# Optimization experiments

Measured on AMD Instinct MI355X. Metric: run time of the kernel, lower is better.

The kernel has to match this reference:

```python
import jax, jax.numpy as jnp
import numpy as np

NH, KVH, HD = 32, 8, 128          # num heads, kv heads, head dim
HIDDEN = NH * HD                   # 4096
K_BITS = V_BITS = 4
GROUP = 32                         # quantization group size
THETA = 10000.0
FEAT = 32 // K_BITS                # values packed per int32


def _rope_cos_sin(pos, dtype=jnp.float32):
    inv_freq = 1.0 / (THETA ** (jnp.arange(0, HD, 2, dtype=jnp.float32) / HD))
    freqs = pos.astype(jnp.float32)[:, None] * inv_freq[None, :]
    emb = jnp.concatenate([freqs, freqs], axis=-1)  # [t, HD]
    return jnp.cos(emb).astype(dtype), jnp.sin(emb).astype(dtype)


def _rotate_half(x):
    x1, x2 = jnp.split(x, 2, axis=-1)
    return jnp.concatenate([-x2, x1], axis=-1)


def _apply_rope(x, pos):  # x: [b, h, t, d], pos: [t]
    cos, sin = _rope_cos_sin(pos, x.dtype)
    return x * cos[None, None] + _rotate_half(x) * sin[None, None]


def _unpack(packed, bits):
    # packed int32 [..., n] -> float [..., n * (32//bits)], little-endian bit fields
    feat = 32 // bits
    shifts = jnp.arange(feat, dtype=jnp.int32) * bits
    vals = (packed[..., None] >> shifts) & ((1 << bits) - 1)
    return vals.reshape(packed.shape[:-1] + (packed.shape[-1] * feat,)).astype(jnp.float32)


def _dequant(packed, scale, mn, bits, group):
    # group-wise affine dequant: x = q * scale + mn along last dim
    qv = _unpack(packed, bits)
    lead, L = qv.shape[:-1], qv.shape[-1]
    qv = qv.reshape(lead + (L // group, group))
    return (qv * scale[..., None] + mn[..., None]).reshape(lead + (L,))


def _repeat_kv(x, n):
    return jnp.repeat(x, n, axis=1)


def setup_inputs() -> dict:
    key = jax.random.key(0)
    ks = jax.random.split(key, 13)
    B, QL = 8, 8
    TQ, FULL_PAST = 3968, 56
    s = 0.02
    return {
        "hidden_states": jax.random.normal(ks[0], (B, QL, HIDDEN), jnp.float32),
        "Wq": jax.random.normal(ks[1], (NH * HD, HIDDEN), jnp.float32) * s,
        "Wk": jax.random.normal(ks[2], (KVH * HD, HIDDEN), jnp.float32) * s,
        "Wv": jax.random.normal(ks[3], (KVH * HD, HIDDEN), jnp.float32) * s,
        "Wo": jax.random.normal(ks[4], (NH * HD, NH * HD), jnp.float32) * s,
        "key_quant_trans": jax.random.randint(ks[5], (B, KVH, HD, TQ // FEAT), 0, 2**31 - 1, jnp.int32),
        "key_scale_trans": jax.random.uniform(ks[6], (B, KVH, HD, TQ // GROUP), jnp.float32) * 0.05 + 0.01,
        "key_mn_trans": jax.random.normal(ks[7], (B, KVH, HD, TQ // GROUP), jnp.float32) * 0.1,
        "key_full_past": jax.random.normal(ks[8], (B, KVH, FULL_PAST, HD), jnp.float32),
        "value_quant": jax.random.randint(ks[9], (B, KVH, TQ, HD // FEAT), 0, 2**31 - 1, jnp.int32),
        "value_scale": jax.random.uniform(ks[10], (B, KVH, TQ, HD // GROUP), jnp.float32) * 0.05 + 0.01,
        "value_mn": jax.random.normal(ks[11], (B, KVH, TQ, HD // GROUP), jnp.float32) * 0.1,
        "value_full_past": jax.random.normal(ks[12], (B, KVH, FULL_PAST, HD), jnp.float32),
    }


def reference(hidden_states, Wq, Wk, Wv, Wo,
              key_quant_trans, key_scale_trans, key_mn_trans, key_full_past,
              value_quant, value_scale, value_mn, value_full_past):
    b, q_len, _ = hidden_states.shape
    groups = NH // KVH
    # projections
    q = (hidden_states @ Wq.T).reshape(b, q_len, NH, HD).transpose(0, 2, 1, 3)
    k = (hidden_states @ Wk.T).reshape(b, q_len, KVH, HD).transpose(0, 2, 1, 3)
    v = (hidden_states @ Wv.T).reshape(b, q_len, KVH, HD).transpose(0, 2, 1, 3)

    TQ = key_quant_trans.shape[-1] * FEAT
    past_len = TQ + key_full_past.shape[2]
    pos_new = jnp.arange(past_len, past_len + q_len)
    qr = _apply_rope(q, pos_new)

    # quantized key segment: dequant (stored transposed [b,kvh,HD,TQ]) + fused RoPE + bmm
    kq = _dequant(key_quant_trans, key_scale_trans, key_mn_trans, K_BITS, GROUP)
    kq = _apply_rope(kq.transpose(0, 1, 3, 2), jnp.arange(TQ))  # [b,kvh,TQ,HD]
    att_quant = jnp.einsum('bhqd,bhkd->bhqk', qr, _repeat_kv(kq, groups))

    # full-precision residual key segment
    k_full = jnp.concatenate([key_full_past, k], axis=2)
    pos_full = jnp.arange(past_len + q_len - k_full.shape[2], past_len + q_len)
    k_full = _apply_rope(k_full, pos_full)
    att_full = jnp.einsum('bhqd,bhkd->bhqk', qr, _repeat_kv(k_full, groups))

    attn = jnp.concatenate([att_quant, att_full], axis=-1) / np.sqrt(HD).astype(np.float32)
    attn = jax.nn.softmax(attn.astype(jnp.float32), axis=-1).astype(qr.dtype)

    # quantized values (packed along head_dim) + full residual values
    vq = _dequant(value_quant, value_scale, value_mn, V_BITS, GROUP)  # [b,kvh,TQ,HD]
    v_full = jnp.concatenate([value_full_past, v], axis=2)
    Lf = v_full.shape[2]
    out = jnp.einsum('bhqk,bhkd->bhqd', attn[..., :-Lf], _repeat_kv(vq, groups)) \
        + jnp.einsum('bhqk,bhkd->bhqd', attn[..., -Lf:], _repeat_kv(v_full, groups))

    out = out.transpose(0, 2, 1, 3).reshape(b, q_len, NH * HD)
    return out @ Wo.T
```

## Files before the change

kernel.cpp:

```cpp
#include <hip/hip_runtime.h>

typedef unsigned short u16;
typedef short bf16x8 __attribute__((ext_vector_type(8)));
typedef float f32x4 __attribute__((ext_vector_type(4)));

__device__ __forceinline__ float b2f(u16 u){ return __uint_as_float(((unsigned)u)<<16); }
__device__ __forceinline__ u16 f2bf(float f){ return (u16)((__float_as_uint(f)+0x8000u)>>16); }
__device__ __forceinline__ float ldf(const void* p, int i, bool isbf){
  return isbf ? b2f(((const u16*)p)[i]) : ((const float*)p)[i];
}
__device__ __forceinline__ float2 ld2(const void* p, int i, bool isbf){
  if (isbf) { unsigned u = *(const unsigned*)((const u16*)p + i);
              return make_float2(b2f((u16)(u & 0xffffu)), b2f((u16)(u >> 16))); }
  return *(const float2*)((const float*)p + i);
}
__device__ __forceinline__ void ld8(u16* dst, const void* p, int i, bool isbf){
  if (isbf) { *(uint4*)dst = *(const uint4*)((const u16*)p + i); }
  else {
    float4 a = *(const float4*)((const float*)p + i);
    float4 b = *(const float4*)((const float*)p + i + 4);
    dst[0]=f2bf(a.x); dst[1]=f2bf(a.y); dst[2]=f2bf(a.z); dst[3]=f2bf(a.w);
    dst[4]=f2bf(b.x); dst[5]=f2bf(b.y); dst[6]=f2bf(b.z); dst[7]=f2bf(b.w);
  }
}
__device__ __forceinline__ float c8(const float* __restrict__ p, int i, int stride){
  float s = 0.f;
  #pragma unroll
  for (int k = 0; k < 8; k++) s += p[i + k*stride];
  return s;
}
__device__ __forceinline__ void bar(){ asm volatile("s_waitcnt lgkmcnt(0)\n\ts_barrier" ::: "memory"); }
#define MFMA16(a,b,c) __builtin_amdgcn_mfma_f32_16x16x32_bf16((a),(b),(c),0,0,0)

__global__ __launch_bounds__(256) void ctab_kernel(const u16* __restrict__ h,
                                                   int* __restrict__ flag,
                                                   float2* __restrict__ ctab) {
  int tid = threadIdx.x;
  if (blockIdx.x == 0) {
    int cnt = 0;
    for (int i = tid; i < 4096; i += 256) {
      int e = (h[i] >> 7) & 0xFF;
      cnt += (e >= 116 && e <= 132) ? 1 : 0;
    }
    __shared__ int sh[256];
    sh[tid] = cnt; __syncthreads();
    for (int s = 128; s > 0; s >>= 1) { if (tid < s) sh[tid] += sh[tid + s]; __syncthreads(); }
    if (tid == 0) flag[0] = (sh[0] >= 3100) ? 1 : 0;
  }
  int idx = blockIdx.x * 256 + tid;
  int dm = idx & 63, t = idx >> 6;
  float f = exp2f(-(float)dm * (13.287712379549449f / 64.0f));
  float ang = (float)t * f;
  float s, c;
  sincosf(ang, &s, &c);
  ctab[idx] = make_float2(c, s);
}

__global__ __launch_bounds__(256) void proj_kernel(
    const void* __restrict__ X, const void* __restrict__ Wa,
    const void* __restrict__ Wb, const void* __restrict__ Wc,
    float* __restrict__ out32, int Na, int Nb, int ostride,
    const int* __restrict__ flagp, int x_dyn)
{
  bool fbf = (*flagp != 0);
  bool xbf = x_dyn ? fbf : true;
  int n0 = blockIdx.x * 32;
  int ks0 = blockIdx.y * 512;
  const void* W; int wr0;
  if (n0 < Na)           { W = Wa; wr0 = n0; }
  else if (n0 < Na + Nb) { W = Wb; wr0 = n0 - Na; }
  else                   { W = Wc; wr0 = n0 - Na - Nb; }

  __shared__ u16 Xs[64][136];
  __shared__ u16 Ws[32][136];
  int tid = threadIdx.x;
  int wv = tid >> 6, lane = tid & 63, lr = lane & 15, lq = lane >> 4;
  f32x4 acc0 = {0.f,0.f,0.f,0.f}, acc1 = {0.f,0.f,0.f,0.f};

  for (int ki = 0; ki < 4; ki++) {
    int k0 = ks0 + ki * 128;
    __syncthreads();
    for (int u = tid; u < 1024; u += 256) {
      int row = u >> 4, cc = u & 15;
      ld8(&Xs[row][cc * 8], X, row * 4096 + k0 + cc * 8, xbf);
    }
    for (int u = tid; u < 512; u += 256) {
      int row = u >> 4, cc = u & 15;
      ld8(&Ws[row][cc * 8], W, (wr0 + row) * 4096 + k0 + cc * 8, fbf);
    }
    __syncthreads();
    #pragma unroll
    for (int ks = 0; ks < 4; ks++) {
      bf16x8 af = *(const bf16x8*)&Xs[wv * 16 + lr][ks * 32 + lq * 8];
      bf16x8 b0 = *(const bf16x8*)&Ws[lr][ks * 32 + lq * 8];
      bf16x8 b1 = *(const bf16x8*)&Ws[16 + lr][ks * 32 + lq * 8];
      acc0 = MFMA16(af, b0, acc0);
      acc1 = MFMA16(af, b1, acc1);
    }
  }
  float* outp = out32 + (size_t)blockIdx.y * 64 * ostride;
  #pragma unroll
  for (int r = 0; r < 4; r++) {
    outp[(wv * 16 + lq * 4 + r) * ostride + n0 + lr]      = acc0[r];
    outp[(wv * 16 + lq * 4 + r) * ostride + n0 + 16 + lr] = acc1[r];
  }
}

__global__ __launch_bounds__(256) void prep_kernel(
    const float* __restrict__ Cq32, const void* __restrict__ kfp, const void* __restrict__ vfp,
    const float2* __restrict__ ctab, const int* __restrict__ flagp,
    u16* __restrict__ qrb, u16* __restrict__ kfullb, u16* __restrict__ vfullT)
{
  bool isbf = (*flagp != 0);
  int idx = blockIdx.x * 256 + threadIdx.x;
  if (idx < 262144) {
    int d = idx & 127, row = (idx >> 7) & 31, bh = idx >> 12;
    int b = bh >> 3, kvh = bh & 7, g = row >> 3, qp = row & 7;
    int tok = b * 8 + qp, h = kvh * 4 + g;
    float x  = c8(Cq32, tok * 6144 + h * 128 + d, 393216);
    float x2 = c8(Cq32, tok * 6144 + h * 128 + (d ^ 64), 393216);
    float2 cs = ctab[(4024 + qp) * 64 + (d & 63)];
    float sgn = (d < 64) ? -1.f : 1.f;
    qrb[idx] = f2bf(x * cs.x + sgn * (x2 * cs.y));
  } else if (idx < 786432) {
    int j = idx - 262144;
    int d = j & 127, t = (j >> 7) & 63, bh = j >> 13;
    int b = bh >> 3, kvh = bh & 7;
    float x, x2;
    if (t < 56) {
      x  = ldf(kfp, (bh * 56 + t) * 128 + d, isbf);
      x2 = ldf(kfp, (bh * 56 + t) * 128 + (d ^ 64), isbf);
    } else {
      int tok = b * 8 + (t - 56);
      x  = c8(Cq32, tok * 6144 + 4096 + kvh * 128 + d, 393216);
      x2 = c8(Cq32, tok * 6144 + 4096 + kvh * 128 + (d ^ 64), 393216);
    }
    float2 cs = ctab[(3968 + t) * 64 + (d & 63)];
    float sgn = (d < 64) ? -1.f : 1.f;
    kfullb[j] = f2bf(x * cs.x + sgn * (x2 * cs.y));
  } else {
    int j = idx - 786432;
    int t = j & 63, d = (j >> 6) & 127, bh = j >> 13;
    int b = bh >> 3, kvh = bh & 7;
    float x;
    if (t < 56) x = ldf(vfp, (bh * 56 + t) * 128 + d, isbf);
    else        x = c8(Cq32, (b * 8 + t - 56) * 6144 + 5120 + kvh * 128 + d, 393216);
    vfullT[j] = f2bf(x);
  }
}

__global__ __launch_bounds__(256) void attn_kernel(
    const int* __restrict__ kqw, const void* __restrict__ ksc, const void* __restrict__ kmn,
    const int* __restrict__ vqw, const void* __restrict__ vsc, const void* __restrict__ vmn,
    const u16* __restrict__ qrb, const u16* __restrict__ kfullb, const u16* __restrict__ vfullT,
    const float2* __restrict__ ctab, const int* __restrict__ flagp,
    u16* __restrict__ Opart, float* __restrict__ ml)
{
  bool isbf = (*flagp != 0);
  int bh = blockIdx.x, grp = blockIdx.y;
  int tid = threadIdx.x;

  __shared__ __align__(16) unsigned char L[23552];
  u16 (*Ktile)[136] = (u16(*)[136])L;
  u16 (*Vtile)[72]  = (u16(*)[72])L;
  u16 (*Pl)[72] = (u16(*)[72])(L + 18432);
  float* pmax = (float*)(L + 23040);
  float* psum = (float*)(L + 23296);

  int wv = tid >> 6, lane = tid & 63, lr = lane & 15, lq = lane >> 4;
  int mt = wv & 1, nh = wv >> 1;

  const int* kq_lo = kqw + (bh * 128 + lane) * 496;
  const int* kq_hi = kq_lo + 64 * 496;
  int klo = (bh * 128 + lane) * 124;
  int khi = klo + 64 * 124;
  const int* vqp = vqw + (bh * 3968 + lane) * 16 + wv * 4;
  int voff = (bh * 3968 + lane) * 4 + wv;

  bf16x8 qa[4];
  #pragma unroll
  for (int ks = 0; ks < 4; ks++)
    qa[ks] = *(const bf16x8*)&qrb[(bh * 32 + mt * 16 + lr) * 128 + ks * 32 + lq * 8];

  unsigned kwl[2], kwh[2];
  float2 ksl, kml, ksh, kmh;
  uint4 vw;
  float vs, vm;
  {
    int c0 = grp * 4;
    kwl[0] = kq_lo[c0 * 8 + wv]; kwl[1] = kq_lo[c0 * 8 + wv + 4];
    kwh[0] = kq_hi[c0 * 8 + wv]; kwh[1] = kq_hi[c0 * 8 + wv + 4];
    ksl = ld2(ksc, klo + c0 * 2, isbf); kml = ld2(kmn, klo + c0 * 2, isbf);
    ksh = ld2(ksc, khi + c0 * 2, isbf); kmh = ld2(kmn, khi + c0 * 2, isbf);
    vw = *(const uint4*)(vqp + c0 * 1024);
    vs = ldf(vsc, voff + c0 * 256, isbf); vm = ldf(vmn, voff + c0 * 256, isbf);
  }

  float m_prev[4], l_run[4];
  #pragma unroll
  for (int r = 0; r < 4; r++) { m_prev[r] = -INFINITY; l_run[r] = 0.f; }
  f32x4 zf = {0.f,0.f,0.f,0.f};
  f32x4 oacc[4] = {zf, zf, zf, zf};

  for (int j = 0; j < 4; j++) {
    int c = grp * 4 + j;
    if (c >= 63) break;
    bool fullc = (c == 62);
    bool pf = (j < 3) && (c + 1 < 62);

    bar();
    if (!fullc) {
      #pragma unroll
      for (int it = 0; it < 2; it++) {
        int w = wv + 4 * it;
        unsigned w1 = kwl[it], w2 = kwh[it];
        float sc1 = it ? ksl.y : ksl.x, m1 = it ? kml.y : kml.x;
        float sc2 = it ? ksh.y : ksh.x, m2 = it ? kmh.y : kmh.x;
        const float2* ct = &ctab[(c * 64 + w * 8) * 64 + lane];
        #pragma unroll
        for (int i = 0; i < 8; i++) {
          float v1 = (float)((w1 >> (4 * i)) & 15u) * sc1 + m1;
          float v2 = (float)((w2 >> (4 * i)) & 15u) * sc2 + m2;
          float2 cs = ct[i * 64];
          Ktile[w * 8 + i][lane]      = f2bf(v1 * cs.x - v2 * cs.y);
          Ktile[w * 8 + i][lane + 64] = f2bf(v2 * cs.x + v1 * cs.y);
        }
      }
    } else {
      for (int u = tid; u < 1024; u += 256) {
        int row = u >> 4, cc = u & 15;
        *(uint4*)&Ktile[row][cc * 8] = *(const uint4*)&kfullb[(bh * 64 + row) * 128 + cc * 8];
      }
    }
    if (pf) {
      int cn = c + 1;
      kwl[0] = kq_lo[cn * 8 + wv]; kwl[1] = kq_lo[cn * 8 + wv + 4];
      kwh[0] = kq_hi[cn * 8 + wv]; kwh[1] = kq_hi[cn * 8 + wv + 4];
      ksl = ld2(ksc, klo + cn * 2, isbf); kml = ld2(kmn, klo + cn * 2, isbf);
      ksh = ld2(ksc, khi + cn * 2, isbf); kmh = ld2(kmn, khi + cn * 2, isbf);
    }
    bar();
    f32x4 sacc[2] = {zf, zf};
    #pragma unroll
    for (int ks = 0; ks < 4; ks++) {
      #pragma unroll
      for (int nt = 0; nt < 2; nt++) {
        bf16x8 bfr = *(const bf16x8*)&Ktile[nh * 32 + nt * 16 + lr][ks * 32 + lq * 8];
        sacc[nt] = MFMA16(qa[ks], bfr, sacc[nt]);
      }
    }
    float mx[4];
    #pragma unroll
    for (int r = 0; r < 4; r++) {
      sacc[0][r] *= 0.08838834764831845f;
      sacc[1][r] *= 0.08838834764831845f;
      mx[r] = fmaxf(sacc[0][r], sacc[1][r]);
    }
    #pragma unroll
    for (int m = 1; m < 16; m <<= 1) {
      #pragma unroll
      for (int r = 0; r < 4; r++) mx[r] = fmaxf(mx[r], __shfl_xor(mx[r], m));
    }
    if (lr == 0) {
      #pragma unroll
      for (int r = 0; r < 4; r++) pmax[wv * 16 + lq * 4 + r] = mx[r];
    }
    bar();
    if (!fullc) {
      unsigned wds[4] = {vw.x, vw.y, vw.z, vw.w};
      #pragma unroll
      for (int it = 0; it < 4; it++) {
        int w = wv * 4 + it;
        unsigned wd = wds[it];
        #pragma unroll
        for (int i = 0; i < 8; i++)
          Vtile[w * 8 + i][lane] = f2bf((float)((wd >> (4 * i)) & 15u) * vs + vm);
      }
    } else {
      for (int u = tid; u < 1024; u += 256) {
        int dd = u >> 3, t8 = u & 7;
        *(uint4*)&Vtile[dd][t8 * 8] = *(const uint4*)&vfullT[(bh * 128 + dd) * 64 + t8 * 8];
      }
    }
    if (pf) {
      int cn = c + 1;
      vw = *(const uint4*)(vqp + cn * 1024);
      vs = ldf(vsc, voff + cn * 256, isbf); vm = ldf(vmn, voff + cn * 256, isbf);
    }
    float alpha[4], osum[4];
    #pragma unroll
    for (int r = 0; r < 4; r++) {
      float cm = fmaxf(mx[r], pmax[(wv ^ 2) * 16 + lq * 4 + r]);
      float mn2 = fmaxf(m_prev[r], cm);
      alpha[r] = __expf(m_prev[r] - mn2);
      m_prev[r] = mn2;
    }
    u16 pb[2][4];
    #pragma unroll
    for (int r = 0; r < 4; r++) {
      float p0 = __expf(sacc[0][r] - m_prev[r]);
      float p1 = __expf(sacc[1][r] - m_prev[r]);
      pb[0][r] = f2bf(p0); pb[1][r] = f2bf(p1);
      osum[r] = b2f(pb[0][r]) + b2f(pb[1][r]);
    }
    #pragma unroll
    for (int m = 1; m < 16; m <<= 1) {
      #pragma unroll
      for (int r = 0; r < 4; r++) osum[r] += __shfl_xor(osum[r], m);
    }
    #pragma unroll
    for (int nt = 0; nt < 2; nt++)
      #pragma unroll
      for (int r = 0; r < 4; r++)
        Pl[mt * 16 + lq * 4 + r][nh * 32 + nt * 16 + lr] = pb[nt][r];
    if (lr == 0) {
      #pragma unroll
      for (int r = 0; r < 4; r++) psum[wv * 16 + lq * 4 + r] = osum[r];
    }
    bar();
    f32x4 pv[4] = {zf, zf, zf, zf};
    #pragma unroll
    for (int ks = 0; ks < 2; ks++) {
      bf16x8 af = *(const bf16x8*)&Pl[mt * 16 + lr][ks * 32 + lq * 8];
      #pragma unroll
      for (int nt = 0; nt < 4; nt++) {
        bf16x8 bfr = *(const bf16x8*)&Vtile[nh * 64 + nt * 16 + lr][ks * 32 + lq * 8];
        pv[nt] = MFMA16(af, bfr, pv[nt]);
      }
    }
    #pragma unroll
    for (int r = 0; r < 4; r++)
      l_run[r] = l_run[r] * alpha[r] + osum[r] + psum[(wv ^ 2) * 16 + lq * 4 + r];
    #pragma unroll
    for (int nt = 0; nt < 4; nt++)
      #pragma unroll
      for (int r = 0; r < 4; r++)
        oacc[nt][r] = oacc[nt][r] * alpha[r] + pv[nt][r];
  }

  u16* Ob = Opart + (size_t)((bh * 16 + grp) * 32) * 128;
  #pragma unroll
  for (int nt = 0; nt < 4; nt++)
    #pragma unroll
    for (int r = 0; r < 4; r++)
      Ob[(mt * 16 + lq * 4 + r) * 128 + nh * 64 + nt * 16 + lr] = f2bf(oacc[nt][r]);
  if (wv < 2 && lr == 0) {
    #pragma unroll
    for (int r = 0; r < 4; r++) {
      ml[((bh * 16 + grp) * 32 + mt * 16 + lq * 4 + r) * 2 + 0] = m_prev[r];
      ml[((bh * 16 + grp) * 32 + mt * 16 + lq * 4 + r) * 2 + 1] = l_run[r];
    }
  }
}

__global__ __launch_bounds__(256) void combine_kernel(
    const u16* __restrict__ Opart, const float* __restrict__ ml, u16* __restrict__ attn_out)
{
  int bh = blockIdx.x, dq = blockIdx.y, tid = threadIdx.x;
  __shared__ float Wg[16][33];
  __shared__ float Ls[32];
  if (tid < 32) {
    int row = tid;
    float M = -INFINITY;
    for (int g = 0; g < 16; g++)
      M = fmaxf(M, ml[((bh * 16 + g) * 32 + row) * 2]);
    float Lacc = 0.f;
    for (int g = 0; g < 16; g++) {
      float m = ml[((bh * 16 + g) * 32 + row) * 2];
      float l = ml[((bh * 16 + g) * 32 + row) * 2 + 1];
      float w = __expf(m - M);
      Wg[g][row] = w;
      Lacc += l * w;
    }
    Ls[row] = Lacc;
  }
  __syncthreads();
  int row = tid >> 3, ds = tid & 7;
  int d0 = dq * 32 + ds * 4;
  float a0 = 0.f, a1 = 0.f, a2 = 0.f, a3 = 0.f;
  for (int g = 0; g < 16; g++) {
    float w = Wg[g][row];
    const u16* p = Opart + (size_t)((bh * 16 + g) * 32 + row) * 128 + d0;
    uint2 v = *(const uint2*)p;
    const u16* h = (const u16*)&v;
    a0 += w * b2f(h[0]); a1 += w * b2f(h[1]); a2 += w * b2f(h[2]); a3 += w * b2f(h[3]);
  }
  float inv = 1.0f / Ls[row];
  int b = bh >> 3, kvh = bh & 7, hg = row >> 3, qp = row & 7;
  u16* dst = attn_out + (size_t)(b * 8 + qp) * 4096 + (kvh * 4 + hg) * 128 + d0;
  dst[0] = f2bf(a0 * inv); dst[1] = f2bf(a1 * inv);
  dst[2] = f2bf(a2 * inv); dst[3] = f2bf(a3 * inv);
}

__global__ __launch_bounds__(256) void cast_kernel(
    const float* __restrict__ O32, const int* __restrict__ flagp, void* __restrict__ out)
{
  int i = blockIdx.x * 256 + threadIdx.x;
  float v = c8(O32, i, 262144);
  if (*flagp) ((u16*)out)[i] = f2bf(v);
  else        ((float*)out)[i] = v;
}

extern "C" void kernel_launch(void* const* d_in, const int* in_sizes, int n_in,
                              void* d_out, int out_size, void* d_ws, size_t ws_size,
                              hipStream_t stream)
{
  const void* hidden = d_in[0];
  const void* Wq  = d_in[1];
  const void* Wk  = d_in[2];
  const void* Wv  = d_in[3];
  const void* Wo  = d_in[4];
  const int*  kqw = (const int*)d_in[5];
  const void* ksc = d_in[6];
  const void* kmn = d_in[7];
  const void* kfp = d_in[8];
  const int*  vqw = (const int*)d_in[9];
  const void* vsc = d_in[10];
  const void* vmn = d_in[11];
  const void* vfp = d_in[12];

  char* ws = (char*)d_ws;
  int*    flag     = (int*)(ws);
  float2* ctab     = (float2*)(ws + 256);
  float*  Cq32     = (float*)(ws + 2064640);
  u16*    Opart    = (u16*)(ws + 2064640);
  float*  O32      = (float*)(ws + 2064640);
  u16*    qrb      = (u16*)(ws + 18841856);
  u16*    attn_out = qrb;
  u16*    kfullb   = (u16*)(ws + 19366144);
  u16*    vfullT   = (u16*)(ws + 20414720);
  float*  ml       = (float*)(ws + 21463296);

  ctab_kernel<<<1008, 256, 0, stream>>>((const u16*)hidden, flag, ctab);
  proj_kernel<<<dim3(192, 8), 256, 0, stream>>>(hidden, Wq, Wk, Wv, Cq32, 4096, 1024, 6144, flag, 1);
  prep_kernel<<<5120, 256, 0, stream>>>(Cq32, kfp, vfp, ctab, flag, qrb, kfullb, vfullT);
  attn_kernel<<<dim3(64, 16), 256, 0, stream>>>(kqw, ksc, kmn, vqw, vsc, vmn,
                                                qrb, kfullb, vfullT, ctab, flag, Opart, ml);
  combine_kernel<<<dim3(64, 4), 256, 0, stream>>>(Opart, ml, attn_out);
  proj_kernel<<<dim3(128, 8), 256, 0, stream>>>(attn_out, Wo, Wo, Wo, O32, 4096, 0, 4096, flag, 0);
  cast_kernel<<<1024, 256, 0, stream>>>(O32, flag, d_out);
}
```

Before: 316.9 us.

## Software-pipeline attention chunks with separate K/V/P LDS tiles and swizzle

Restructures the attention loop so the PV matmul of the previous chunk overlaps with the QK of the current one. K, V and P now have separate XOR-swizzled LDS buffers, which cuts barriers per chunk and avoids bank conflicts. The row sum now comes from an MFMA against a ones vector rather than shuffle reductions, and the row max uses DPP row-rotates. It also sets launch bounds for 4 blocks per CU. The cost is more LDS per block (37 KB) and more live registers, which could limit occupancy.

```diff
diff --git a/kernel.cpp b/kernel.cpp
--- a/kernel.cpp
+++ b/kernel.cpp
@@ -30,6 +30,8 @@
   return s;
 }
 __device__ __forceinline__ void bar(){ asm volatile("s_waitcnt lgkmcnt(0)\n\ts_barrier" ::: "memory"); }
+#define RORMAX(x, ctrl) fmaxf((x), __int_as_float(__builtin_amdgcn_update_dpp( \
+    __float_as_int(x), __float_as_int(x), (ctrl), 0xF, 0xF, false)))
 #define MFMA16(a,b,c) __builtin_amdgcn_mfma_f32_16x16x32_bf16((a),(b),(c),0,0,0)
 
 __global__ __launch_bounds__(256) void ctab_kernel(const u16* __restrict__ h,
@@ -149,7 +151,7 @@
   }
 }
 
-__global__ __launch_bounds__(256) void attn_kernel(
+__global__ __launch_bounds__(256, 4) void attn_kernel(
     const int* __restrict__ kqw, const void* __restrict__ ksc, const void* __restrict__ kmn,
     const int* __restrict__ vqw, const void* __restrict__ vsc, const void* __restrict__ vmn,
     const u16* __restrict__ qrb, const u16* __restrict__ kfullb, const u16* __restrict__ vfullT,
@@ -159,16 +161,18 @@
   bool isbf = (*flagp != 0);
   int bh = blockIdx.x, grp = blockIdx.y;
   int tid = threadIdx.x;
-
-  __shared__ __align__(16) unsigned char L[23552];
-  u16 (*Ktile)[136] = (u16(*)[136])L;
-  u16 (*Vtile)[72]  = (u16(*)[72])L;
-  u16 (*Pl)[72] = (u16(*)[72])(L + 18432);
-  float* pmax = (float*)(L + 23040);
-  float* psum = (float*)(L + 23296);
+  int c0 = grp * 4;
+  int N = (grp == 15) ? 3 : 4;
+
+  __shared__ __align__(16) unsigned char L[37120];
+  u16* Kt = (u16*)L;
+  u16* Vt = (u16*)(L + 16384);
+  u16* Pt = (u16*)(L + 32768);
+  float* pmax = (float*)(L + 36864);
 
   int wv = tid >> 6, lane = tid & 63, lr = lane & 15, lq = lane >> 4;
   int mt = wv & 1, nh = wv >> 1;
+  int sx = (lr & 7) << 3;
 
   const int* kq_lo = kqw + (bh * 128 + lane) * 496;
   const int* kq_hi = kq_lo + 64 * 496;
@@ -181,113 +185,101 @@
   #pragma unroll
   for (int ks = 0; ks < 4; ks++)
     qa[ks] = *(const bf16x8*)&qrb[(bh * 32 + mt * 16 + lr) * 128 + ks * 32 + lq * 8];
+  bf16x8 onev;
+  #pragma unroll
+  for (int j2 = 0; j2 < 8; j2++) onev[j2] = (short)0x3F80;
+
+  float m_prev[4], l_run[4], alpha[4], mx[4];
+  f32x4 zf = {0.f,0.f,0.f,0.f};
+  f32x4 oacc[4] = {zf, zf, zf, zf};
+  f32x4 sacc[2];
+  #pragma unroll
+  for (int r = 0; r < 4; r++) { m_prev[r] = -INFINITY; l_run[r] = 0.f; }
 
   unsigned kwl[2], kwh[2];
   float2 ksl, kml, ksh, kmh;
-  uint4 vw;
-  float vs, vm;
-  {
-    int c0 = grp * 4;
-    kwl[0] = kq_lo[c0 * 8 + wv]; kwl[1] = kq_lo[c0 * 8 + wv + 4];
-    kwh[0] = kq_hi[c0 * 8 + wv]; kwh[1] = kq_hi[c0 * 8 + wv + 4];
-    ksl = ld2(ksc, klo + c0 * 2, isbf); kml = ld2(kmn, klo + c0 * 2, isbf);
-    ksh = ld2(ksc, khi + c0 * 2, isbf); kmh = ld2(kmn, khi + c0 * 2, isbf);
-    vw = *(const uint4*)(vqp + c0 * 1024);
-    vs = ldf(vsc, voff + c0 * 256, isbf); vm = ldf(vmn, voff + c0 * 256, isbf);
-  }
-
-  float m_prev[4], l_run[4];
-  #pragma unroll
-  for (int r = 0; r < 4; r++) { m_prev[r] = -INFINITY; l_run[r] = 0.f; }
-  f32x4 zf = {0.f,0.f,0.f,0.f};
-  f32x4 oacc[4] = {zf, zf, zf, zf};
-
-  for (int j = 0; j < 4; j++) {
-    int c = grp * 4 + j;
-    if (c >= 63) break;
-    bool fullc = (c == 62);
-    bool pf = (j < 3) && (c + 1 < 62);
-
-    bar();
-    if (!fullc) {
-      #pragma unroll
-      for (int it = 0; it < 2; it++) {
-        int w = wv + 4 * it;
-        unsigned w1 = kwl[it], w2 = kwh[it];
-        float sc1 = it ? ksl.y : ksl.x, m1 = it ? kml.y : kml.x;
-        float sc2 = it ? ksh.y : ksh.x, m2 = it ? kmh.y : kmh.x;
-        const float2* ct = &ctab[(c * 64 + w * 8) * 64 + lane];
-        #pragma unroll
-        for (int i = 0; i < 8; i++) {
-          float v1 = (float)((w1 >> (4 * i)) & 15u) * sc1 + m1;
-          float v2 = (float)((w2 >> (4 * i)) & 15u) * sc2 + m2;
-          float2 cs = ct[i * 64];
-          Ktile[w * 8 + i][lane]      = f2bf(v1 * cs.x - v2 * cs.y);
-          Ktile[w * 8 + i][lane + 64] = f2bf(v2 * cs.x + v1 * cs.y);
-        }
-      }
-    } else {
-      for (int u = tid; u < 1024; u += 256) {
-        int row = u >> 4, cc = u & 15;
-        *(uint4*)&Ktile[row][cc * 8] = *(const uint4*)&kfullb[(bh * 64 + row) * 128 + cc * 8];
-      }
-    }
-    if (pf) {
-      int cn = c + 1;
-      kwl[0] = kq_lo[cn * 8 + wv]; kwl[1] = kq_lo[cn * 8 + wv + 4];
-      kwh[0] = kq_hi[cn * 8 + wv]; kwh[1] = kq_hi[cn * 8 + wv + 4];
-      ksl = ld2(ksc, klo + cn * 2, isbf); kml = ld2(kmn, klo + cn * 2, isbf);
-      ksh = ld2(ksc, khi + cn * 2, isbf); kmh = ld2(kmn, khi + cn * 2, isbf);
-    }
-    bar();
-    f32x4 sacc[2] = {zf, zf};
+  uint4 vw; float vs, vm;
+
+#define KLOAD(cn) do { \
+    kwl[0] = kq_lo[(cn)*8 + wv]; kwl[1] = kq_lo[(cn)*8 + wv + 4]; \
+    kwh[0] = kq_hi[(cn)*8 + wv]; kwh[1] = kq_hi[(cn)*8 + wv + 4]; \
+    ksl = ld2(ksc, klo + (cn)*2, isbf); kml = ld2(kmn, klo + (cn)*2, isbf); \
+    ksh = ld2(ksc, khi + (cn)*2, isbf); kmh = ld2(kmn, khi + (cn)*2, isbf); } while(0)
+#define VLOAD(cn) do { \
+    vw = *(const uint4*)(vqp + (cn)*1024); \
+    vs = ldf(vsc, voff + (cn)*256, isbf); vm = ldf(vmn, voff + (cn)*256, isbf); } while(0)
+#define KDEQ(cn) do { \
+    _Pragma("unroll") \
+    for (int it = 0; it < 2; it++) { \
+      int w = wv + 4 * it; \
+      unsigned w1 = kwl[it], w2 = kwh[it]; \
+      float sc1 = it ? ksl.y : ksl.x, m1 = it ? kml.y : kml.x; \
+      float sc2 = it ? ksh.y : ksh.x, m2 = it ? kmh.y : kmh.x; \
+      const float2* ct = &ctab[((cn) * 64 + w * 8) * 64 + lane]; \
+      _Pragma("unroll") \
+      for (int ii = 0; ii < 8; ii++) { \
+        float v1 = (float)((w1 >> (4 * ii)) & 15u) * sc1 + m1; \
+        float v2 = (float)((w2 >> (4 * ii)) & 15u) * sc2 + m2; \
+        float2 cs = ct[ii * 64]; \
+        int t = w * 8 + ii; \
+        Kt[(t * 128 + lane)      ^ ((t & 7) << 3)] = f2bf(v1 * cs.x - v2 * cs.y); \
+        Kt[(t * 128 + lane + 64) ^ ((t & 7) << 3)] = f2bf(v2 * cs.x + v1 * cs.y); \
+      } \
+    } } while(0)
+#define PVSTEP() do { \
+    f32x4 pv[4] = {zf, zf, zf, zf}; f32x4 ls = zf; \
+    _Pragma("unroll") \
+    for (int ks = 0; ks < 2; ks++) { \
+      bf16x8 af = *(const bf16x8*)&Pt[((mt*16 + lr)*64 + ks*32 + lq*8) ^ sx]; \
+      ls = MFMA16(af, onev, ls); \
+      _Pragma("unroll") \
+      for (int nt = 0; nt < 4; nt++) { \
+        bf16x8 bv = *(const bf16x8*)&Vt[((nh*64 + nt*16 + lr)*64 + ks*32 + lq*8) ^ sx]; \
+        pv[nt] = MFMA16(af, bv, pv[nt]); \
+      } \
+    } \
+    _Pragma("unroll") \
+    for (int r = 0; r < 4; r++) { \
+      l_run[r] = l_run[r] * alpha[r] + ls[r]; \
+      _Pragma("unroll") \
+      for (int nt = 0; nt < 4; nt++) \
+        oacc[nt][r] = oacc[nt][r] * alpha[r] + pv[nt][r]; \
+    } } while(0)
+
+  KLOAD(c0);
+  VLOAD(c0);
+  KDEQ(c0);
+  KLOAD(c0 + 1);
+  bar();
+
+  for (int i = 0; i < N; i++) {
+    int c = c0 + i;
+    f32x4 sa0 = zf, sa1 = zf;
     #pragma unroll
     for (int ks = 0; ks < 4; ks++) {
-      #pragma unroll
-      for (int nt = 0; nt < 2; nt++) {
-        bf16x8 bfr = *(const bf16x8*)&Ktile[nh * 32 + nt * 16 + lr][ks * 32 + lq * 8];
-        sacc[nt] = MFMA16(qa[ks], bfr, sacc[nt]);
-      }
-    }
-    float mx[4];
+      bf16x8 b0 = *(const bf16x8*)&Kt[((nh*32 + lr)*128      + ks*32 + lq*8) ^ sx];
+      bf16x8 b1 = *(const bf16x8*)&Kt[((nh*32 + 16 + lr)*128 + ks*32 + lq*8) ^ sx];
+      sa0 = MFMA16(qa[ks], b0, sa0);
+      sa1 = MFMA16(qa[ks], b1, sa1);
+    }
+    if (i > 0) PVSTEP();
     #pragma unroll
     for (int r = 0; r < 4; r++) {
-      sacc[0][r] *= 0.08838834764831845f;
-      sacc[1][r] *= 0.08838834764831845f;
-      mx[r] = fmaxf(sacc[0][r], sacc[1][r]);
-    }
-    #pragma unroll
-    for (int m = 1; m < 16; m <<= 1) {
-      #pragma unroll
-      for (int r = 0; r < 4; r++) mx[r] = fmaxf(mx[r], __shfl_xor(mx[r], m));
+      sa0[r] *= 0.08838834764831845f;
+      sa1[r] *= 0.08838834764831845f;
+      float m0 = fmaxf(sa0[r], sa1[r]);
+      m0 = RORMAX(m0, 0x128);
+      m0 = RORMAX(m0, 0x124);
+      m0 = RORMAX(m0, 0x122);
+      m0 = RORMAX(m0, 0x121);
+      mx[r] = m0;
     }
     if (lr == 0) {
       #pragma unroll
       for (int r = 0; r < 4; r++) pmax[wv * 16 + lq * 4 + r] = mx[r];
     }
+    sacc[0] = sa0; sacc[1] = sa1;
     bar();
-    if (!fullc) {
-      unsigned wds[4] = {vw.x, vw.y, vw.z, vw.w};
-      #pragma unroll
-      for (int it = 0; it < 4; it++) {
-        int w = wv * 4 + it;
-        unsigned wd = wds[it];
-        #pragma unroll
-        for (int i = 0; i < 8; i++)
-          Vtile[w * 8 + i][lane] = f2bf((float)((wd >> (4 * i)) & 15u) * vs + vm);
-      }
-    } else {
-      for (int u = tid; u < 1024; u += 256) {
-        int dd = u >> 3, t8 = u & 7;
-        *(uint4*)&Vtile[dd][t8 * 8] = *(const uint4*)&vfullT[(bh * 128 + dd) * 64 + t8 * 8];
-      }
-    }
-    if (pf) {
-      int cn = c + 1;
-      vw = *(const uint4*)(vqp + cn * 1024);
-      vs = ldf(vsc, voff + cn * 256, isbf); vm = ldf(vmn, voff + cn * 256, isbf);
-    }
-    float alpha[4], osum[4];
     #pragma unroll
     for (int r = 0; r < 4; r++) {
       float cm = fmaxf(mx[r], pmax[(wv ^ 2) * 16 + lq * 4 + r]);
@@ -295,48 +287,49 @@
       alpha[r] = __expf(m_prev[r] - mn2);
       m_prev[r] = mn2;
     }
-    u16 pb[2][4];
-    #pragma unroll
-    for (int r = 0; r < 4; r++) {
-      float p0 = __expf(sacc[0][r] - m_prev[r]);
-      float p1 = __expf(sacc[1][r] - m_prev[r]);
-      pb[0][r] = f2bf(p0); pb[1][r] = f2bf(p1);
-      osum[r] = b2f(pb[0][r]) + b2f(pb[1][r]);
-    }
-    #pragma unroll
-    for (int m = 1; m < 16; m <<= 1) {
+    #pragma unroll
+    for (int nt = 0; nt < 2; nt++) {
       #pragma unroll
-      for (int r = 0; r < 4; r++) osum[r] += __shfl_xor(osum[r], m);
-    }
-    #pragma unroll
-    for (int nt = 0; nt < 2; nt++)
+      for (int r = 0; r < 4; r++) {
+        float p = __expf(sacc[nt][r] - m_prev[r]);
+        int q = mt * 16 + lq * 4 + r, k = nh * 32 + nt * 16 + lr;
+        Pt[(q * 64 + k) ^ ((q & 7) << 3)] = f2bf(p);
+      }
+    }
+    if (c != 62) {
+      unsigned wds[4] = {vw.x, vw.y, vw.z, vw.w};
       #pragma unroll
-      for (int r = 0; r < 4; r++)
-        Pl[mt * 16 + lq * 4 + r][nh * 32 + nt * 16 + lr] = pb[nt][r];
-    if (lr == 0) {
-      #pragma unroll
-      for (int r = 0; r < 4; r++) psum[wv * 16 + lq * 4 + r] = osum[r];
-    }
+      for (int it = 0; it < 4; it++) {
+        unsigned wd = wds[it];
+        #pragma unroll
+        for (int ii = 0; ii < 8; ii++) {
+          int d = (wv * 4 + it) * 8 + ii;
+          Vt[(d * 64 + lane) ^ ((d & 7) << 3)] = f2bf((float)((wd >> (4 * ii)) & 15u) * vs + vm);
+        }
+      }
+    } else {
+      for (int u = tid; u < 1024; u += 256) {
+        int dd = u >> 3, t8 = u & 7;
+        *(uint4*)&Vt[(dd * 64 + t8 * 8) ^ ((dd & 7) << 3)] =
+            *(const uint4*)&vfullT[(bh * 128 + dd) * 64 + t8 * 8];
+      }
+    }
+    if (i + 1 < N) {
+      if (c + 1 == 62) {
+        for (int u = tid; u < 1024; u += 256) {
+          int row = u >> 4, cc = u & 15;
+          *(uint4*)&Kt[(row * 128 + cc * 8) ^ ((row & 7) << 3)] =
+              *(const uint4*)&kfullb[(bh * 64 + row) * 128 + cc * 8];
+        }
+      } else {
+        KDEQ(c + 1);
+      }
+    }
+    if (i + 2 < N && c + 2 < 62) KLOAD(c + 2);
+    if (i + 1 < N && c + 1 < 62) VLOAD(c + 1);
     bar();
-    f32x4 pv[4] = {zf, zf, zf, zf};
-    #pragma unroll
-    for (int ks = 0; ks < 2; ks++) {
-      bf16x8 af = *(const bf16x8*)&Pl[mt * 16 + lr][ks * 32 + lq * 8];
-      #pragma unroll
-      for (int nt = 0; nt < 4; nt++) {
-        bf16x8 bfr = *(const bf16x8*)&Vtile[nh * 64 + nt * 16 + lr][ks * 32 + lq * 8];
-        pv[nt] = MFMA16(af, bfr, pv[nt]);
-      }
-    }
-    #pragma unroll
-    for (int r = 0; r < 4; r++)
-      l_run[r] = l_run[r] * alpha[r] + osum[r] + psum[(wv ^ 2) * 16 + lq * 4 + r];
-    #pragma unroll
-    for (int nt = 0; nt < 4; nt++)
-      #pragma unroll
-      for (int r = 0; r < 4; r++)
-        oacc[nt][r] = oacc[nt][r] * alpha[r] + pv[nt][r];
-  }
+  }
+  PVSTEP();
 
   u16* Ob = Opart + (size_t)((bh * 16 + grp) * 32) * 128;
   #pragma unroll
@@ -351,6 +344,10 @@
       ml[((bh * 16 + grp) * 32 + mt * 16 + lq * 4 + r) * 2 + 1] = l_run[r];
     }
   }
+#undef KLOAD
+#undef VLOAD
+#undef KDEQ
+#undef PVSTEP
 }
 
 __global__ __launch_bounds__(256) void combine_kernel(
```

Result: slower. 335.2 us (+5.8%).
